# Optimization experiments

Measured on AMD Instinct MI355X. Metric: run time of the kernel, lower is better.

The kernel has to match this reference:

```python
import jax, jax.numpy as jnp
import numpy as np

V, DW, D, H, F, N = 50272, 512, 1024, 16, 4096, 4   # vocab, word_embed_proj_dim, hidden, heads, ffn, layers
B, L = 4, 1024
T = B * L
MAX_POS = 2048


def layernorm(x, w, b, eps=1e-5):
    m = jnp.mean(x, axis=-1, keepdims=True)
    v = jnp.mean((x - m) ** 2, axis=-1, keepdims=True)
    return (x - m) * jax.lax.rsqrt(v + eps) * w + b


def setup_inputs() -> dict:
    key = jax.random.key(0)
    ks = jax.random.split(key, 16)
    s = 0.02
    inp = {
        "input_ids": jax.random.randint(ks[0], (T,), 0, V),
        "positions": jnp.tile(jnp.arange(L), B),          # per-sequence positions 0..L-1
        "offsets": (jnp.arange(B) + 1) * L,               # cumulative sequence ends
        "cache_indices": jnp.arange(T),
        "k_cache": jnp.zeros((N, T, D), jnp.float32),
        "v_cache": jnp.zeros((N, T, D), jnp.float32),
        "embed_w": jax.random.normal(ks[1], (V, DW)) * s,
        "pos_w": jax.random.normal(ks[2], (MAX_POS + 2, D)) * s,
        "proj_in_w": jax.random.normal(ks[3], (D, DW)) * s,
        "proj_out_w": jax.random.normal(ks[4], (DW, D)) * s,
        "ln1_w": jnp.ones((N, D)), "ln1_b": jnp.zeros((N, D)),
        "qw": jax.random.normal(ks[5], (N, D, D)) * s, "qb": jnp.zeros((N, D)),
        "kw": jax.random.normal(ks[6], (N, D, D)) * s, "kb": jnp.zeros((N, D)),
        "vw": jax.random.normal(ks[7], (N, D, D)) * s, "vb": jnp.zeros((N, D)),
        "ow": jax.random.normal(ks[8], (N, D, D)) * s, "ob": jnp.zeros((N, D)),
        "fc1w": jax.random.normal(ks[9], (N, F, D)) * s, "fc1b": jnp.zeros((N, F)),
        "fc2w": jax.random.normal(ks[10], (N, D, F)) * s, "fc2b": jnp.zeros((N, D)),
        "ln2_w": jnp.ones((N, D)), "ln2_b": jnp.zeros((N, D)),
    }
    return inp


def reference(input_ids, positions, offsets, cache_indices, k_cache, v_cache,
              embed_w, pos_w, proj_in_w, proj_out_w,
              ln1_w, ln1_b, qw, qb, kw, kb, vw, vb, ow, ob,
              fc1w, fc1b, fc2w, fc2b, ln2_w, ln2_b):
    # prompt_init=True path: fresh causal varlen attention over packed equal-length sequences.
    hd = D // H
    scale = hd ** -0.5
    emb = embed_w[input_ids] @ proj_in_w.T            # [T, D] (proj_in since DW != D)
    pos = pos_w[positions + 2]                        # learned pos emb with offset 2
    h = (emb + pos).reshape(B, L, D)
    causal = jnp.tril(jnp.ones((L, L), bool))

    def step(h, p):
        l1w, l1b, Wq, bq, Wk, bk, Wv, bv, Wo, bo, W1, b1, W2, b2, l2w, l2b = p
        r = h                                          # post-LN (do_layer_norm_before=False)
        q = (h @ Wq.T + bq).reshape(B, L, H, hd)
        k = (h @ Wk.T + bk).reshape(B, L, H, hd)
        v = (h @ Wv.T + bv).reshape(B, L, H, hd)
        s = jnp.einsum('bqhd,bkhd->bhqk', q * scale, k)
        s = jnp.where(causal, s, -1e9)
        pa = jax.nn.softmax(s, axis=-1)
        o = jnp.einsum('bhqk,bkhd->bqhd', pa, v).reshape(B, L, D)
        h = layernorm(r + (o @ Wo.T + bo), l1w, l1b)
        r = h
        h = jax.nn.relu(h @ W1.T + b1)
        h = h @ W2.T + b2
        h = layernorm(r + h, l2w, l2b)
        return h, None

    h, _ = jax.lax.scan(step, h, (ln1_w, ln1_b, qw, qb, kw, kb, vw, vb, ow, ob,
                                  fc1w, fc1b, fc2w, fc2b, ln2_w, ln2_b))
    # no decoder final_layer_norm when do_layer_norm_before=False
    h = h.reshape(T, D) @ proj_out_w.T                # [T, DW]
    last = h[offsets - 1]                             # last token of each sequence [B, DW]
    return last @ embed_w.T                           # logits [B, V]
```

## Files before the change

### kernel.cpp

```cpp
#include <hip/hip_runtime.h>
#include <stdint.h>

typedef _Float16 f16;
typedef __attribute__((ext_vector_type(8))) _Float16 f16x8;
typedef __attribute__((ext_vector_type(4))) _Float16 f16x4;
typedef __attribute__((ext_vector_type(4))) float f32x4;

constexpr int kT = 4096;
constexpr int kD = 1024;
constexpr int kDW = 512;
constexpr int kF = 4096;
constexpr int kV = 50272;

__device__ __forceinline__ void gload16(const void* g, void* lbase, int lane) {
#if __has_builtin(__builtin_amdgcn_global_load_lds)
  __builtin_amdgcn_global_load_lds((const __attribute__((address_space(1))) void*)g,
                                   (__attribute__((address_space(3))) void*)lbase, 16, 0, 0);
#else
  *(f16x8*)((char*)lbase + lane * 16) = *(const f16x8*)g;
#endif
}

__global__ __launch_bounds__(512, 4) void gemm_p8(
    const f16* __restrict__ A, const f16* __restrict__ W,
    const float* __restrict__ bias, void* __restrict__ Cv,
    int M, int N, int K, int ldc, int flags, int S)
{
  __shared__ f16 LA[2][128 * 64];
  __shared__ f16 LB[2][128 * 64];
  const int tid = threadIdx.x, lane = tid & 63, wv = tid >> 6;
  const int nby = M >> 7;
  const int nb = nby * (N >> 7);
  int id = blockIdx.x;
  id = (id & 7) * ((int)gridDim.x >> 3) + (id >> 3);
  const int s = id / nb;
  const int r = id - s * nb;
  const int bx = r / nby, by = r - bx * nby;
  const int row0 = by * 128, col0 = bx * 128;
  const int klen = K / S, koff = s * klen;
  const int wm = (wv >> 1) * 32, wn = (wv & 1) * 64;
  const int l15 = lane & 15, l4 = lane >> 4;

  f32x4 acc[2][4] = {};

  const int srow = wv * 16 + (lane >> 3);
  const int schunk = ((lane & 7) ^ (lane >> 3)) * 8;
  const f16* Ag = A + (size_t)(row0 + srow) * K + koff + schunk;
  const f16* Wg = W + (size_t)(col0 + srow) * K + koff + schunk;
  const int lrow = wv * 16;

  const int nt = klen >> 6;
#pragma unroll
  for (int j = 0; j < 2; ++j) {
    gload16(Ag + (size_t)j * 8 * K, &LA[0][(lrow + j * 8) * 64], lane);
    gload16(Wg + (size_t)j * 8 * K, &LB[0][(lrow + j * 8) * 64], lane);
  }

  for (int t = 0; t < nt; ++t) {
    const int cur = t & 1;
    if (t + 1 < nt) {
      const size_t ko = (size_t)(t + 1) * 64;
#pragma unroll
      for (int j = 0; j < 2; ++j) {
        gload16(Ag + (size_t)j * 8 * K + ko, &LA[cur ^ 1][(lrow + j * 8) * 64], lane);
        gload16(Wg + (size_t)j * 8 * K + ko, &LB[cur ^ 1][(lrow + j * 8) * 64], lane);
      }
      asm volatile("s_waitcnt vmcnt(4)" ::: "memory");
    } else {
      asm volatile("s_waitcnt vmcnt(0)" ::: "memory");
    }
    __builtin_amdgcn_s_barrier();

    f16x8 af[2][2], bf[2][4];
#pragma unroll
    for (int ks = 0; ks < 2; ++ks) {
#pragma unroll
      for (int mr = 0; mr < 2; ++mr) {
        const int rowa = wm + mr * 16 + l15;
        const int csw = (((ks * 4 + l4) ^ (rowa & 7)) * 8);
        af[ks][mr] = *(const f16x8*)&LA[cur][rowa * 64 + csw];
      }
#pragma unroll
      for (int nr = 0; nr < 4; ++nr) {
        const int rowb = wn + nr * 16 + l15;
        const int csw = (((ks * 4 + l4) ^ (rowb & 7)) * 8);
        bf[ks][nr] = *(const f16x8*)&LB[cur][rowb * 64 + csw];
      }
    }
#pragma unroll
    for (int mr = 0; mr < 2; ++mr)
#pragma unroll
      for (int nr = 0; nr < 4; ++nr) {
        acc[mr][nr] = __builtin_amdgcn_mfma_f32_16x16x32_f16(af[0][mr], bf[0][nr], acc[mr][nr], 0, 0, 0);
        acc[mr][nr] = __builtin_amdgcn_mfma_f32_16x16x32_f16(af[1][mr], bf[1][nr], acc[mr][nr], 0, 0, 0);
      }
    __builtin_amdgcn_sched_barrier(0);
    __builtin_amdgcn_s_barrier();
  }

  const bool relu = (flags & 1) != 0;
  const bool outf = (flags & 2) != 0;
  float* Cf = (float*)Cv + (size_t)s * M * ldc;
  f16* Ch = (f16*)Cv;
  const float* bs = (s == 0) ? bias : nullptr;
#pragma unroll
  for (int nr = 0; nr < 4; ++nr) {
    const int col = col0 + wn + nr * 16 + l15;
    const float bv = bs ? bs[col] : 0.f;
#pragma unroll
    for (int mr = 0; mr < 2; ++mr) {
#pragma unroll
      for (int rr = 0; rr < 4; ++rr) {
        const int row = row0 + wm + mr * 16 + l4 * 4 + rr;
        float v = acc[mr][nr][rr] + bv;
        if (relu) v = fmaxf(v, 0.f);
        if (outf) Cf[(size_t)row * ldc + col] = v;
        else      Ch[(size_t)row * ldc + col] = (f16)v;
      }
    }
  }
}

__global__ __launch_bounds__(256) void gemm_f16(
    const f16* __restrict__ A, const float* __restrict__ W,
    const float* __restrict__ bias, void* __restrict__ Cv,
    int M, int N, int K, int ldc, int flags)
{
  __shared__ f16 As[128][40];
  __shared__ f16 Ws[128][40];
  const int tid = threadIdx.x;
  const int lane = tid & 63;
  const int wid = tid >> 6;
  const int row0 = blockIdx.y * 128, col0 = blockIdx.x * 128;
  const int wm = (wid >> 1) * 64, wn = (wid & 1) * 64;
  const int l15 = lane & 15, k8 = (lane >> 4) * 8;
  const int lr = tid >> 2, lc8 = (tid & 3) * 8;

  f32x4 acc[4][4] = {};

  const f16* Ap = A + (size_t)(row0 + lr) * K + lc8;
  const float* Wp = W + (size_t)(col0 + lr) * K + lc8;

  for (int k0 = 0; k0 < K; k0 += 32) {
    f16x8 a0 = *(const f16x8*)(Ap + k0);
    f16x8 a1 = *(const f16x8*)(Ap + (size_t)64 * K + k0);
    f32x4 w00 = *(const f32x4*)(Wp + k0);
    f32x4 w01 = *(const f32x4*)(Wp + k0 + 4);
    f32x4 w10 = *(const f32x4*)(Wp + (size_t)64 * K + k0);
    f32x4 w11 = *(const f32x4*)(Wp + (size_t)64 * K + k0 + 4);
    f16x8 wv0, wv1;
#pragma unroll
    for (int j = 0; j < 4; ++j) {
      wv0[j] = (f16)w00[j]; wv0[4 + j] = (f16)w01[j];
      wv1[j] = (f16)w10[j]; wv1[4 + j] = (f16)w11[j];
    }
    __syncthreads();
    *(f16x8*)&As[lr][lc8] = a0;
    *(f16x8*)&As[lr + 64][lc8] = a1;
    *(f16x8*)&Ws[lr][lc8] = wv0;
    *(f16x8*)&Ws[lr + 64][lc8] = wv1;
    __syncthreads();
    f16x8 af[4], bfr[4];
#pragma unroll
    for (int r = 0; r < 4; ++r) af[r] = *(const f16x8*)&As[wm + r * 16 + l15][k8];
#pragma unroll
    for (int r = 0; r < 4; ++r) bfr[r] = *(const f16x8*)&Ws[wn + r * 16 + l15][k8];
#pragma unroll
    for (int mr = 0; mr < 4; ++mr)
#pragma unroll
      for (int nr = 0; nr < 4; ++nr)
        acc[mr][nr] = __builtin_amdgcn_mfma_f32_16x16x32_f16(af[mr], bfr[nr], acc[mr][nr], 0, 0, 0);
  }

  const bool relu = (flags & 1) != 0;
  const bool outf = (flags & 2) != 0;
  float* Cf = (float*)Cv;
  f16* Ch = (f16*)Cv;
#pragma unroll
  for (int nr = 0; nr < 4; ++nr) {
    const int col = col0 + wn + nr * 16 + l15;
    const float bv = bias ? bias[col] : 0.f;
#pragma unroll
    for (int mr = 0; mr < 4; ++mr) {
#pragma unroll
      for (int r = 0; r < 4; ++r) {
        const int row = row0 + wm + mr * 16 + (lane >> 4) * 4 + r;
        float v = acc[mr][nr][r] + bv;
        if (relu) v = fmaxf(v, 0.f);
        if (outf) Cf[(size_t)row * ldc + col] = v;
        else      Ch[(size_t)row * ldc + col] = (f16)v;
      }
    }
  }
}

__global__ __launch_bounds__(256) void attn_mfma(const f16* __restrict__ qkv,
                                                 f16* __restrict__ out)
{
  __shared__ f16 Ks[64][72];
  __shared__ f16 Vt[64][72];
  __shared__ f16 Ps[4][16][72];
  const int qt = blockIdx.x, h = blockIdx.y, b = blockIdx.z;
  const int tid = threadIdx.x, lane = tid & 63, wv = tid >> 6;
  const int l15 = lane & 15, l4 = lane >> 4;

  const size_t qrow = (size_t)(b * 1024 + qt * 64 + wv * 16 + l15);
  const f16* qp = qkv + qrow * 3072 + h * 64 + l4 * 8;
  const f16x8 qa0 = *(const f16x8*)qp;
  const f16x8 qa1 = *(const f16x8*)(qp + 32);

  float m[4] = {-1e30f, -1e30f, -1e30f, -1e30f};
  float l[4] = {0.f, 0.f, 0.f, 0.f};
  f32x4 o[4] = {};

  const int skey = tid >> 2;
  const int spart = (tid & 3) * 16;

  for (int kt = 0; kt <= qt; ++kt) {
    __syncthreads();
    {
      const f16* kvb = qkv + (size_t)(b * 1024 + kt * 64 + skey) * 3072 + h * 64;
      f16x8 kk0 = *(const f16x8*)(kvb + 1024 + spart);
      f16x8 kk1 = *(const f16x8*)(kvb + 1024 + spart + 8);
      f16x8 vv0 = *(const f16x8*)(kvb + 2048 + spart);
      f16x8 vv1 = *(const f16x8*)(kvb + 2048 + spart + 8);
      *(f16x8*)&Ks[skey][spart] = kk0;
      *(f16x8*)&Ks[skey][spart + 8] = kk1;
#pragma unroll
      for (int j = 0; j < 8; ++j) {
        Vt[spart + j][skey] = vv0[j];
        Vt[spart + 8 + j][skey] = vv1[j];
      }
    }
    __syncthreads();

    f32x4 s[4] = {};
#pragma unroll
    for (int f = 0; f < 4; ++f) {
      f16x8 kb0 = *(const f16x8*)&Ks[f * 16 + l15][l4 * 8];
      f16x8 kb1 = *(const f16x8*)&Ks[f * 16 + l15][32 + l4 * 8];
      s[f] = __builtin_amdgcn_mfma_f32_16x16x32_f16(qa0, kb0, s[f], 0, 0, 0);
      s[f] = __builtin_amdgcn_mfma_f32_16x16x32_f16(qa1, kb1, s[f], 0, 0, 0);
    }
    float sc[4][4];
    if (kt == qt) {
#pragma unroll
      for (int f = 0; f < 4; ++f)
#pragma unroll
        for (int r = 0; r < 4; ++r) {
          const int qg = wv * 16 + l4 * 4 + r;
          const int kg = f * 16 + l15;
          sc[f][r] = (kg <= qg) ? s[f][r] * 0.125f : -1e9f;
        }
    } else {
#pragma unroll
      for (int f = 0; f < 4; ++f)
#pragma unroll
        for (int r = 0; r < 4; ++r) sc[f][r] = s[f][r] * 0.125f;
    }
    float corr[4];
#pragma unroll
    for (int r = 0; r < 4; ++r) {
      float tm = fmaxf(fmaxf(sc[0][r], sc[1][r]), fmaxf(sc[2][r], sc[3][r]));
      tm = fmaxf(tm, __shfl_xor(tm, 1));
      tm = fmaxf(tm, __shfl_xor(tm, 2));
      tm = fmaxf(tm, __shfl_xor(tm, 4));
      tm = fmaxf(tm, __shfl_xor(tm, 8));
      const float mn = fmaxf(m[r], tm);
      corr[r] = __expf(m[r] - mn);
      float ps = 0.f;
#pragma unroll
      for (int f = 0; f < 4; ++f) { sc[f][r] = __expf(sc[f][r] - mn); ps += sc[f][r]; }
      ps += __shfl_xor(ps, 1);
      ps += __shfl_xor(ps, 2);
      ps += __shfl_xor(ps, 4);
      ps += __shfl_xor(ps, 8);
      l[r] = l[r] * corr[r] + ps;
      m[r] = mn;
    }
#pragma unroll
    for (int f = 0; f < 4; ++f)
#pragma unroll
      for (int r = 0; r < 4; ++r)
        Ps[wv][l4 * 4 + r][f * 16 + l15] = (f16)sc[f][r];
#pragma unroll
    for (int hf = 0; hf < 4; ++hf)
#pragma unroll
      for (int r = 0; r < 4; ++r) o[hf][r] *= corr[r];
    f16x8 pa0 = *(const f16x8*)&Ps[wv][l15][l4 * 8];
    f16x8 pa1 = *(const f16x8*)&Ps[wv][l15][32 + l4 * 8];
#pragma unroll
    for (int hf = 0; hf < 4; ++hf) {
      f16x8 vb0 = *(const f16x8*)&Vt[hf * 16 + l15][l4 * 8];
      f16x8 vb1 = *(const f16x8*)&Vt[hf * 16 + l15][32 + l4 * 8];
      o[hf] = __builtin_amdgcn_mfma_f32_16x16x32_f16(pa0, vb0, o[hf], 0, 0, 0);
      o[hf] = __builtin_amdgcn_mfma_f32_16x16x32_f16(pa1, vb1, o[hf], 0, 0, 0);
    }
  }

  float inv[4];
#pragma unroll
  for (int r = 0; r < 4; ++r) inv[r] = 1.f / l[r];
  f16* dst = out + (size_t)(b * 1024 + qt * 64 + wv * 16 + l4 * 4) * 1024 + h * 64 + l15;
#pragma unroll
  for (int hf = 0; hf < 4; ++hf)
#pragma unroll
    for (int r = 0; r < 4; ++r)
      dst[(size_t)r * 1024 + hf * 16] = (f16)(o[hf][r] * inv[r]);
}

__global__ __launch_bounds__(256) void add_ln3(
    const float* __restrict__ R, const float* __restrict__ X1,
    const float* __restrict__ X2,
    const float* __restrict__ w, const float* __restrict__ bvec,
    float* __restrict__ O32, f16* __restrict__ Oh)
{
  const int row = blockIdx.x, tid = threadIdx.x;
  const size_t base = (size_t)row * 1024 + tid * 4;
  f32x4 v = *(const f32x4*)&R[base];
  v += *(const f32x4*)&X1[base];
  v += *(const f32x4*)&X2[base];
  float sm = v[0] + v[1] + v[2] + v[3];
  float sq = v[0] * v[0] + v[1] * v[1] + v[2] * v[2] + v[3] * v[3];
#pragma unroll
  for (int msk = 32; msk; msk >>= 1) { sm += __shfl_xor(sm, msk); sq += __shfl_xor(sq, msk); }
  __shared__ float sb[4], qb_[4];
  const int wid = tid >> 6, lane = tid & 63;
  if (lane == 0) { sb[wid] = sm; qb_[wid] = sq; }
  __syncthreads();
  sm = sb[0] + sb[1] + sb[2] + sb[3];
  sq = qb_[0] + qb_[1] + qb_[2] + qb_[3];
  const float mean = sm * (1.f / 1024.f);
  const float var = sq * (1.f / 1024.f) - mean * mean;
  const float rstd = rsqrtf(var + 1e-5f);
  const f32x4 w4 = *(const f32x4*)&w[tid * 4];
  const f32x4 b4 = *(const f32x4*)&bvec[tid * 4];
  f32x4 y;
  f16x4 yh;
#pragma unroll
  for (int j = 0; j < 4; ++j) {
    y[j] = (v[j] - mean) * rstd * w4[j] + b4[j];
    yh[j] = (f16)y[j];
  }
  *(f32x4*)&O32[base] = y;
  *(f16x4*)&Oh[base] = yh;
}

__global__ __launch_bounds__(256) void add_ln(
    const float* __restrict__ R, const float* __restrict__ X,
    const float* __restrict__ w, const float* __restrict__ bvec,
    float* __restrict__ O32, f16* __restrict__ Oh)
{
  const int row = blockIdx.x, tid = threadIdx.x;
  const size_t base = (size_t)row * 1024 + tid * 4;
  f32x4 v = *(const f32x4*)&R[base];
  v += *(const f32x4*)&X[base];
  float sm = v[0] + v[1] + v[2] + v[3];
  float sq = v[0] * v[0] + v[1] * v[1] + v[2] * v[2] + v[3] * v[3];
#pragma unroll
  for (int msk = 32; msk; msk >>= 1) { sm += __shfl_xor(sm, msk); sq += __shfl_xor(sq, msk); }
  __shared__ float sb[4], qb_[4];
  const int wid = tid >> 6, lane = tid & 63;
  if (lane == 0) { sb[wid] = sm; qb_[wid] = sq; }
  __syncthreads();
  sm = sb[0] + sb[1] + sb[2] + sb[3];
  sq = qb_[0] + qb_[1] + qb_[2] + qb_[3];
  const float mean = sm * (1.f / 1024.f);
  const float var = sq * (1.f / 1024.f) - mean * mean;
  const float rstd = rsqrtf(var + 1e-5f);
  const f32x4 w4 = *(const f32x4*)&w[tid * 4];
  const f32x4 b4 = *(const f32x4*)&bvec[tid * 4];
  f32x4 y;
  f16x4 yh;
#pragma unroll
  for (int j = 0; j < 4; ++j) {
    y[j] = (v[j] - mean) * rstd * w4[j] + b4[j];
    yh[j] = (f16)y[j];
  }
  *(f32x4*)&O32[base] = y;
  *(f16x4*)&Oh[base] = yh;
}

__global__ __launch_bounds__(256) void gather_embed(
    const int* __restrict__ ids, const float* __restrict__ ew, f16* __restrict__ E)
{
  const int idx = blockIdx.x * 256 + threadIdx.x;
  const int t = idx >> 6, c = (idx & 63) * 8;
  const float* src = ew + (size_t)ids[t] * 512 + c;
  f32x4 f0 = *(const f32x4*)src, f1 = *(const f32x4*)(src + 4);
  f16x8 o_;
#pragma unroll
  for (int j = 0; j < 4; ++j) { o_[j] = (f16)f0[j]; o_[4 + j] = (f16)f1[j]; }
  *(f16x8*)(E + (size_t)t * 512 + c) = o_;
}

__global__ __launch_bounds__(256) void pos_add2(
    const float* __restrict__ X1, const float* __restrict__ X2,
    const float* __restrict__ posw,
    const int* __restrict__ positions, float* __restrict__ H32, f16* __restrict__ Hh)
{
  const int idx = blockIdx.x * 256 + threadIdx.x;
  const int t = idx >> 7, c = (idx & 127) * 8;
  const size_t base = (size_t)t * 1024 + c;
  const float* pp = posw + (size_t)(positions[t] + 2) * 1024 + c;
  f32x4 a0 = *(const f32x4*)&X1[base];
  f32x4 a1 = *(const f32x4*)&X1[base + 4];
  a0 += *(const f32x4*)&X2[base];
  a1 += *(const f32x4*)&X2[base + 4];
  a0 += *(const f32x4*)pp;
  a1 += *(const f32x4*)(pp + 4);
  f16x8 hh;
#pragma unroll
  for (int j = 0; j < 4; ++j) { hh[j] = (f16)a0[j]; hh[4 + j] = (f16)a1[j]; }
  *(f32x4*)&H32[base] = a0;
  *(f32x4*)&H32[base + 4] = a1;
  *(f16x8*)&Hh[base] = hh;
}

__global__ __launch_bounds__(256) void pos_add(
    const float* __restrict__ X, const float* __restrict__ posw,
    const int* __restrict__ positions, float* __restrict__ H32, f16* __restrict__ Hh)
{
  const int idx = blockIdx.x * 256 + threadIdx.x;
  const int t = idx >> 7, c = (idx & 127) * 8;
  const float* xp = X + (size_t)t * 1024 + c;
  const float* pp = posw + (size_t)(positions[t] + 2) * 1024 + c;
  f32x4 a0 = *(const f32x4*)xp, a1 = *(const f32x4*)(xp + 4);
  a0 += *(const f32x4*)pp;
  a1 += *(const f32x4*)(pp + 4);
  f16x8 hh;
#pragma unroll
  for (int j = 0; j < 4; ++j) { hh[j] = (f16)a0[j]; hh[4 + j] = (f16)a1[j]; }
  *(f32x4*)&H32[(size_t)t * 1024 + c] = a0;
  *(f32x4*)&H32[(size_t)t * 1024 + c + 4] = a1;
  *(f16x8*)&Hh[(size_t)t * 1024 + c] = hh;
}

__global__ __launch_bounds__(256) void last_proj(
    const float* __restrict__ H32, const float* __restrict__ pw,
    const int* __restrict__ offs, float* __restrict__ y)
{
  const int o = blockIdx.x * 4 + (threadIdx.x >> 6), lane = threadIdx.x & 63;
  const int b = o >> 9, w = o & 511;
  const int row = offs[b] - 1;
  const float* hp = H32 + (size_t)row * 1024;
  const float* wp = pw + (size_t)w * 1024;
  float s = 0.f;
#pragma unroll
  for (int j = 0; j < 4; ++j) {
    f32x4 hv = *(const f32x4*)&hp[(lane + 64 * j) * 4];
    f32x4 wv = *(const f32x4*)&wp[(lane + 64 * j) * 4];
    s += hv[0] * wv[0] + hv[1] * wv[1] + hv[2] * wv[2] + hv[3] * wv[3];
  }
#pragma unroll
  for (int msk = 32; msk; msk >>= 1) s += __shfl_xor(s, msk);
  if (lane == 0) y[o] = s;
}

__global__ __launch_bounds__(256) void logits4(const float* __restrict__ y,
                                               const float* __restrict__ ew,
                                               float* __restrict__ out)
{
  __shared__ float ys[2048];
  const int tid = threadIdx.x;
  ((f32x4*)ys)[tid] = ((const f32x4*)y)[tid];
  ((f32x4*)ys)[tid + 256] = ((const f32x4*)y)[tid + 256];
  __syncthreads();
  const int v = blockIdx.x * 4 + (tid >> 6);
  const int lane = tid & 63;
  const float* wp = ew + (size_t)v * 512 + lane * 8;
  const f32x4 e0 = *(const f32x4*)wp;
  const f32x4 e1 = *(const f32x4*)(wp + 4);
  float s0 = 0.f, s1 = 0.f, s2 = 0.f, s3 = 0.f;
#pragma unroll
  for (int j = 0; j < 4; ++j) {
    const int c0 = lane * 8 + j, c1 = lane * 8 + 4 + j;
    s0 += e0[j] * ys[c0] + e1[j] * ys[c1];
    s1 += e0[j] * ys[512 + c0] + e1[j] * ys[512 + c1];
    s2 += e0[j] * ys[1024 + c0] + e1[j] * ys[1024 + c1];
    s3 += e0[j] * ys[1536 + c0] + e1[j] * ys[1536 + c1];
  }
#pragma unroll
  for (int msk = 32; msk; msk >>= 1) {
    s0 += __shfl_xor(s0, msk); s1 += __shfl_xor(s1, msk);
    s2 += __shfl_xor(s2, msk); s3 += __shfl_xor(s3, msk);
  }
  if (lane == 0) {
    out[v] = s0;
    out[50272 + v] = s1;
    out[2 * 50272 + v] = s2;
    out[3 * 50272 + v] = s3;
  }
}

__global__ __launch_bounds__(256) void conv_f16(const float* __restrict__ s,
                                                f16* __restrict__ d, int n8)
{
  const int i = blockIdx.x * 256 + threadIdx.x;
  if (i >= n8) return;
  const f32x4 a = *(const f32x4*)(s + (size_t)i * 8);
  const f32x4 b = *(const f32x4*)(s + (size_t)i * 8 + 4);
  f16x8 o_;
#pragma unroll
  for (int j = 0; j < 4; ++j) { o_[j] = (f16)a[j]; o_[4 + j] = (f16)b[j]; }
  *(f16x8*)(d + (size_t)i * 8) = o_;
}

__global__ __launch_bounds__(256) void qkvw_pack(const float* __restrict__ qw,
                                                 const float* __restrict__ kw,
                                                 const float* __restrict__ vw,
                                                 f16* __restrict__ dst)
{
  const size_t i = (size_t)(blockIdx.x * 256 + threadIdx.x) * 8;
  const size_t li = i / 3145728;
  const size_t r = i - li * 3145728;
  const int mt = (int)(r >> 20);
  const size_t c = r & 1048575;
  const float* s = (mt == 0 ? qw : (mt == 1 ? kw : vw)) + li * 1048576 + c;
  const f32x4 a = *(const f32x4*)s;
  const f32x4 b = *(const f32x4*)(s + 4);
  f16x8 o_;
#pragma unroll
  for (int j = 0; j < 4; ++j) { o_[j] = (f16)a[j]; o_[4 + j] = (f16)b[j]; }
  *(f16x8*)(dst + i) = o_;
}

__global__ __launch_bounds__(256) void qkvb_pack(const float* __restrict__ qb,
                                                 const float* __restrict__ kb,
                                                 const float* __restrict__ vb,
                                                 float* __restrict__ dst)
{
  const int i = blockIdx.x * 256 + threadIdx.x;
  const int li = i / 3072;
  const int r = i - li * 3072;
  const int mt = r >> 10;
  const int c = r & 1023;
  const float* s = (mt == 0 ? qb : (mt == 1 ? kb : vb));
  dst[i] = s[li * 1024 + c];
}

extern "C" void kernel_launch(void* const* d_in, const int* in_sizes, int n_in,
                              void* d_out, int out_size, void* d_ws, size_t ws_size,
                              hipStream_t stream)
{
  const int* ids        = (const int*)d_in[0];
  const int* positions  = (const int*)d_in[1];
  const int* offs       = (const int*)d_in[2];
  const float* embed_w    = (const float*)d_in[6];
  const float* pos_w      = (const float*)d_in[7];
  const float* proj_in_w  = (const float*)d_in[8];
  const float* proj_out_w = (const float*)d_in[9];
  const float* ln1w = (const float*)d_in[10];
  const float* ln1b = (const float*)d_in[11];
  const float* qw   = (const float*)d_in[12];
  const float* qb   = (const float*)d_in[13];
  const float* kw   = (const float*)d_in[14];
  const float* kb   = (const float*)d_in[15];
  const float* vw   = (const float*)d_in[16];
  const float* vb   = (const float*)d_in[17];
  const float* ow   = (const float*)d_in[18];
  const float* ob   = (const float*)d_in[19];
  const float* fc1w = (const float*)d_in[20];
  const float* fc1b = (const float*)d_in[21];
  const float* fc2w = (const float*)d_in[22];
  const float* fc2b = (const float*)d_in[23];
  const float* ln2w = (const float*)d_in[24];
  const float* ln2b = (const float*)d_in[25];

  char* ws = (char*)d_ws;
  size_t off = 0;
  auto take = [&](size_t bytes) -> char* {
    char* p = ws + off;
    off += (bytes + 255) & ~(size_t)255;
    return p;
  };
  f16*   E   = (f16*)  take((size_t)kT * kDW * 2);
  float* h32 = (float*)take((size_t)kT * kD * 4);
  f16*   hbf = (f16*)  take((size_t)kT * kD * 2);
  f16*   qkv = (f16*)  take((size_t)kT * 3072 * 2);
  f16*   att = (f16*)  take((size_t)kT * kD * 2);
  f16*   t1  = (f16*)  take((size_t)kT * kF * 2);
  float* t2  = (float*)take((size_t)kT * kD * 4 * 2);
  float* yb  = (float*)take((size_t)4 * kDW * 4);
  f16*   pw_in = (f16*)take((size_t)kD * kDW * 2);
  f16*   qkvw  = (f16*)take((size_t)4 * 3072 * kD * 2);
  f16*   oww   = (f16*)take((size_t)4 * kD * kD * 2);
  f16*   f1w   = (f16*)take((size_t)4 * kF * kD * 2);
  f16*   f2w   = (f16*)take((size_t)4 * kD * kF * 2);
  float* qkvb  = (float*)take((size_t)4 * 3072 * 4);
  const bool wok = (off <= ws_size);
  float* t2b = t2 + (size_t)kT * kD;
  (void)in_sizes; (void)n_in; (void)out_size;

  const dim3 blk(256);
  const dim3 blk8(512);
  const dim3 gD(kD / 128, kT / 128);
  const dim3 gF(kF / 128, kT / 128);
  const dim3 gAtt(16, 16, 4);
  const int nbD   = (kD / 128) * (kT / 128);
  const int nbQKV = (3072 / 128) * (kT / 128);
  const int nbF   = (kF / 128) * (kT / 128);

  if (wok) {
    conv_f16<<<256, blk, 0, stream>>>(proj_in_w, pw_in, 65536);
    qkvw_pack<<<6144, blk, 0, stream>>>(qw, kw, vw, qkvw);
    conv_f16<<<2048, blk, 0, stream>>>(ow, oww, 524288);
    conv_f16<<<8192, blk, 0, stream>>>(fc1w, f1w, 2097152);
    conv_f16<<<8192, blk, 0, stream>>>(fc2w, f2w, 2097152);
    qkvb_pack<<<48, blk, 0, stream>>>(qb, kb, vb, qkvb);
  }

  gather_embed<<<1024, blk, 0, stream>>>(ids, embed_w, E);
  if (wok) {
    gemm_p8<<<nbD * 2, blk8, 0, stream>>>(E, pw_in, nullptr, t2, kT, kD, kDW, kD, 2, 2);
    pos_add2<<<2048, blk, 0, stream>>>(t2, t2b, pos_w, positions, h32, hbf);
  } else {
    gemm_f16<<<gD, blk, 0, stream>>>(E, proj_in_w, nullptr, t2, kT, kD, kDW, kD, 2);
    pos_add<<<2048, blk, 0, stream>>>(t2, pos_w, positions, h32, hbf);
  }

  for (int n = 0; n < 4; ++n) {
    const size_t wo = (size_t)n * kD * kD;
    if (wok) {
      gemm_p8<<<nbQKV, blk8, 0, stream>>>(hbf, qkvw + (size_t)n * 3145728, qkvb + n * 3072,
                                          qkv, kT, 3072, kD, 3072, 0, 1);
      attn_mfma<<<gAtt, blk, 0, stream>>>(qkv, att);
      gemm_p8<<<nbD * 2, blk8, 0, stream>>>(att, oww + wo, ob + n * kD, t2, kT, kD, kD, kD, 2, 2);
      add_ln3<<<kT, blk, 0, stream>>>(h32, t2, t2b, ln1w + n * kD, ln1b + n * kD, h32, hbf);
      gemm_p8<<<nbF, blk8, 0, stream>>>(hbf, f1w + (size_t)n * kF * kD, fc1b + n * kF, t1, kT, kF, kD, kF, 1, 1);
      gemm_p8<<<nbD * 2, blk8, 0, stream>>>(t1, f2w + (size_t)n * kD * kF, fc2b + n * kD, t2, kT, kD, kF, kD, 2, 2);
      add_ln3<<<kT, blk, 0, stream>>>(h32, t2, t2b, ln2w + n * kD, ln2b + n * kD, h32, hbf);
    } else {
      gemm_f16<<<gD, blk, 0, stream>>>(hbf, qw + wo, qb + n * kD, qkv + 0,    kT, kD, kD, 3072, 0);
      gemm_f16<<<gD, blk, 0, stream>>>(hbf, kw + wo, kb + n * kD, qkv + 1024, kT, kD, kD, 3072, 0);
      gemm_f16<<<gD, blk, 0, stream>>>(hbf, vw + wo, vb + n * kD, qkv + 2048, kT, kD, kD, 3072, 0);
      attn_mfma<<<gAtt, blk, 0, stream>>>(qkv, att);
      gemm_f16<<<gD, blk, 0, stream>>>(att, ow + wo, ob + n * kD, t2, kT, kD, kD, kD, 2);
      add_ln<<<kT, blk, 0, stream>>>(h32, t2, ln1w + n * kD, ln1b + n * kD, h32, hbf);
      gemm_f16<<<gF, blk, 0, stream>>>(hbf, fc1w + (size_t)n * kF * kD, fc1b + n * kF, t1, kT, kF, kD, kF, 1);
      gemm_f16<<<gD, blk, 0, stream>>>(t1, fc2w + (size_t)n * kD * kF, fc2b + n * kD, t2, kT, kD, kF, kD, 2);
      add_ln<<<kT, blk, 0, stream>>>(h32, t2, ln2w + n * kD, ln2b + n * kD, h32, hbf);
    }
  }

  last_proj<<<512, blk, 0, stream>>>(h32, proj_out_w, offs, yb);
  logits4<<<12568, blk, 0, stream>>>(yb, embed_w, (float*)d_out);
}
```

Before: 1.202 ms.

## Enlarge attention query tile to 128 rows and swizzle transposed V in LDS

The attention kernel now handles 128 query rows per block, with each wave owning 32 rows as two MFMA row groups. Each K/V tile loaded into shared memory is reused by twice as many queries, which halves K/V global traffic and launches half as many blocks. The transposed V tile gets an XOR swizzle on its column index to reduce LDS bank conflicts. In exchange, causal work is less balanced across waves because some waves skip tiles while others compute, and register pressure rises.

```diff
diff --git a/kernel.cpp b/kernel.cpp
--- a/kernel.cpp
+++ b/kernel.cpp
@@ -194,29 +194,40 @@
   }
 }
 
-__global__ __launch_bounds__(256) void attn_mfma(const f16* __restrict__ qkv,
-                                                 f16* __restrict__ out)
+__global__ __launch_bounds__(256) void attn_mfma2(const f16* __restrict__ qkv,
+                                                  f16* __restrict__ out)
 {
   __shared__ f16 Ks[64][72];
   __shared__ f16 Vt[64][72];
-  __shared__ f16 Ps[4][16][72];
+  __shared__ f16 Ps[4][32][72];
   const int qt = blockIdx.x, h = blockIdx.y, b = blockIdx.z;
   const int tid = threadIdx.x, lane = tid & 63, wv = tid >> 6;
   const int l15 = lane & 15, l4 = lane >> 4;
 
-  const size_t qrow = (size_t)(b * 1024 + qt * 64 + wv * 16 + l15);
-  const f16* qp = qkv + qrow * 3072 + h * 64 + l4 * 8;
-  const f16x8 qa0 = *(const f16x8*)qp;
-  const f16x8 qa1 = *(const f16x8*)(qp + 32);
-
-  float m[4] = {-1e30f, -1e30f, -1e30f, -1e30f};
-  float l[4] = {0.f, 0.f, 0.f, 0.f};
-  f32x4 o[4] = {};
+  f16x8 qa[2][2];
+#pragma unroll
+  for (int mr = 0; mr < 2; ++mr) {
+    const size_t qrow = (size_t)(b * 1024 + qt * 128 + wv * 32 + mr * 16 + l15);
+#pragma unroll
+    for (int ks = 0; ks < 2; ++ks)
+      qa[mr][ks] = *(const f16x8*)(qkv + qrow * 3072 + h * 64 + ks * 32 + l4 * 8);
+  }
+
+  float m[2][4], l[2][4];
+#pragma unroll
+  for (int mr = 0; mr < 2; ++mr)
+#pragma unroll
+    for (int r = 0; r < 4; ++r) { m[mr][r] = -1e30f; l[mr][r] = 0.f; }
+  f32x4 o[2][4] = {};
 
   const int skey = tid >> 2;
   const int spart = (tid & 3) * 16;
-
-  for (int kt = 0; kt <= qt; ++kt) {
+  const int vxor = (skey >> 3) ^ (tid & 3);
+  const int vcol = vxor * 8 + (skey & 7);
+  const int qmin = qt * 128 + wv * 32;
+  const int ntiles = 2 * qt + 2;
+
+  for (int kt = 0; kt < ntiles; ++kt) {
     __syncthreads();
     {
       const f16* kvb = qkv + (size_t)(b * 1024 + kt * 64 + skey) * 3072 + h * 64;
@@ -228,85 +239,104 @@
       *(f16x8*)&Ks[skey][spart + 8] = kk1;
 #pragma unroll
       for (int j = 0; j < 8; ++j) {
-        Vt[spart + j][skey] = vv0[j];
-        Vt[spart + 8 + j][skey] = vv1[j];
+        Vt[spart + j][vcol] = vv0[j];
+        Vt[spart + 8 + j][vcol] = vv1[j];
       }
     }
     __syncthreads();
 
-    f32x4 s[4] = {};
-#pragma unroll
-    for (int f = 0; f < 4; ++f) {
-      f16x8 kb0 = *(const f16x8*)&Ks[f * 16 + l15][l4 * 8];
-      f16x8 kb1 = *(const f16x8*)&Ks[f * 16 + l15][32 + l4 * 8];
-      s[f] = __builtin_amdgcn_mfma_f32_16x16x32_f16(qa0, kb0, s[f], 0, 0, 0);
-      s[f] = __builtin_amdgcn_mfma_f32_16x16x32_f16(qa1, kb1, s[f], 0, 0, 0);
-    }
-    float sc[4][4];
-    if (kt == qt) {
-#pragma unroll
-      for (int f = 0; f < 4; ++f)
+    if (kt * 64 <= qmin + 31) {
+      f32x4 s[2][4] = {};
+#pragma unroll
+      for (int f = 0; f < 4; ++f) {
+        f16x8 kb0 = *(const f16x8*)&Ks[f * 16 + l15][l4 * 8];
+        f16x8 kb1 = *(const f16x8*)&Ks[f * 16 + l15][32 + l4 * 8];
+#pragma unroll
+        for (int mr = 0; mr < 2; ++mr) {
+          s[mr][f] = __builtin_amdgcn_mfma_f32_16x16x32_f16(qa[mr][0], kb0, s[mr][f], 0, 0, 0);
+          s[mr][f] = __builtin_amdgcn_mfma_f32_16x16x32_f16(qa[mr][1], kb1, s[mr][f], 0, 0, 0);
+        }
+      }
+#pragma unroll
+      for (int mr = 0; mr < 2; ++mr) {
+        float sc[4][4];
+        const bool needmask = (kt * 64 + 63) > (qmin + mr * 16);
+        if (needmask) {
+#pragma unroll
+          for (int f = 0; f < 4; ++f)
+#pragma unroll
+            for (int r = 0; r < 4; ++r) {
+              const int qg = qmin + mr * 16 + l4 * 4 + r;
+              const int kg = kt * 64 + f * 16 + l15;
+              sc[f][r] = (kg <= qg) ? s[mr][f][r] * 0.125f : -1e9f;
+            }
+        } else {
+#pragma unroll
+          for (int f = 0; f < 4; ++f)
+#pragma unroll
+            for (int r = 0; r < 4; ++r) sc[f][r] = s[mr][f][r] * 0.125f;
+        }
+        float corr[4];
 #pragma unroll
         for (int r = 0; r < 4; ++r) {
-          const int qg = wv * 16 + l4 * 4 + r;
-          const int kg = f * 16 + l15;
-          sc[f][r] = (kg <= qg) ? s[f][r] * 0.125f : -1e9f;
+          float tm = fmaxf(fmaxf(sc[0][r], sc[1][r]), fmaxf(sc[2][r], sc[3][r]));
+          tm = fmaxf(tm, __shfl_xor(tm, 1));
+          tm = fmaxf(tm, __shfl_xor(tm, 2));
+          tm = fmaxf(tm, __shfl_xor(tm, 4));
+          tm = fmaxf(tm, __shfl_xor(tm, 8));
+          const float mn = fmaxf(m[mr][r], tm);
+          corr[r] = __expf(m[mr][r] - mn);
+          float ps = 0.f;
+#pragma unroll
+          for (int f = 0; f < 4; ++f) { sc[f][r] = __expf(sc[f][r] - mn); ps += sc[f][r]; }
+          ps += __shfl_xor(ps, 1);
+          ps += __shfl_xor(ps, 2);
+          ps += __shfl_xor(ps, 4);
+          ps += __shfl_xor(ps, 8);
+          l[mr][r] = l[mr][r] * corr[r] + ps;
+          m[mr][r] = mn;
         }
-    } else {
-#pragma unroll
-      for (int f = 0; f < 4; ++f)
-#pragma unroll
-        for (int r = 0; r < 4; ++r) sc[f][r] = s[f][r] * 0.125f;
-    }
-    float corr[4];
-#pragma unroll
-    for (int r = 0; r < 4; ++r) {
-      float tm = fmaxf(fmaxf(sc[0][r], sc[1][r]), fmaxf(sc[2][r], sc[3][r]));
-      tm = fmaxf(tm, __shfl_xor(tm, 1));
-      tm = fmaxf(tm, __shfl_xor(tm, 2));
-      tm = fmaxf(tm, __shfl_xor(tm, 4));
-      tm = fmaxf(tm, __shfl_xor(tm, 8));
-      const float mn = fmaxf(m[r], tm);
-      corr[r] = __expf(m[r] - mn);
-      float ps = 0.f;
-#pragma unroll
-      for (int f = 0; f < 4; ++f) { sc[f][r] = __expf(sc[f][r] - mn); ps += sc[f][r]; }
-      ps += __shfl_xor(ps, 1);
-      ps += __shfl_xor(ps, 2);
-      ps += __shfl_xor(ps, 4);
-      ps += __shfl_xor(ps, 8);
-      l[r] = l[r] * corr[r] + ps;
-      m[r] = mn;
-    }
-#pragma unroll
-    for (int f = 0; f < 4; ++f)
+#pragma unroll
+        for (int f = 0; f < 4; ++f)
+#pragma unroll
+          for (int r = 0; r < 4; ++r)
+            Ps[wv][mr * 16 + l4 * 4 + r][f * 16 + l15] = (f16)sc[f][r];
+#pragma unroll
+        for (int hf = 0; hf < 4; ++hf)
+#pragma unroll
+          for (int r = 0; r < 4; ++r) o[mr][hf][r] *= corr[r];
+      }
+      f16x8 pa[2][2];
+#pragma unroll
+      for (int mr = 0; mr < 2; ++mr)
+#pragma unroll
+        for (int ks = 0; ks < 2; ++ks)
+          pa[mr][ks] = *(const f16x8*)&Ps[wv][mr * 16 + l15][ks * 32 + l4 * 8];
+#pragma unroll
+      for (int hf = 0; hf < 4; ++hf) {
+        f16x8 vb0 = *(const f16x8*)&Vt[hf * 16 + l15][((l4) ^ hf) * 8];
+        f16x8 vb1 = *(const f16x8*)&Vt[hf * 16 + l15][((4 + l4) ^ hf) * 8];
+#pragma unroll
+        for (int mr = 0; mr < 2; ++mr) {
+          o[mr][hf] = __builtin_amdgcn_mfma_f32_16x16x32_f16(pa[mr][0], vb0, o[mr][hf], 0, 0, 0);
+          o[mr][hf] = __builtin_amdgcn_mfma_f32_16x16x32_f16(pa[mr][1], vb1, o[mr][hf], 0, 0, 0);
+        }
+      }
+    }
+  }
+
+#pragma unroll
+  for (int mr = 0; mr < 2; ++mr) {
+    float inv[4];
+#pragma unroll
+    for (int r = 0; r < 4; ++r) inv[r] = 1.f / l[mr][r];
+    f16* dst = out + (size_t)(b * 1024 + qt * 128 + wv * 32 + mr * 16 + l4 * 4) * 1024 + h * 64 + l15;
+#pragma unroll
+    for (int hf = 0; hf < 4; ++hf)
 #pragma unroll
       for (int r = 0; r < 4; ++r)
-        Ps[wv][l4 * 4 + r][f * 16 + l15] = (f16)sc[f][r];
-#pragma unroll
-    for (int hf = 0; hf < 4; ++hf)
-#pragma unroll
-      for (int r = 0; r < 4; ++r) o[hf][r] *= corr[r];
-    f16x8 pa0 = *(const f16x8*)&Ps[wv][l15][l4 * 8];
-    f16x8 pa1 = *(const f16x8*)&Ps[wv][l15][32 + l4 * 8];
-#pragma unroll
-    for (int hf = 0; hf < 4; ++hf) {
-      f16x8 vb0 = *(const f16x8*)&Vt[hf * 16 + l15][l4 * 8];
-      f16x8 vb1 = *(const f16x8*)&Vt[hf * 16 + l15][32 + l4 * 8];
-      o[hf] = __builtin_amdgcn_mfma_f32_16x16x32_f16(pa0, vb0, o[hf], 0, 0, 0);
-      o[hf] = __builtin_amdgcn_mfma_f32_16x16x32_f16(pa1, vb1, o[hf], 0, 0, 0);
-    }
-  }
-
-  float inv[4];
-#pragma unroll
-  for (int r = 0; r < 4; ++r) inv[r] = 1.f / l[r];
-  f16* dst = out + (size_t)(b * 1024 + qt * 64 + wv * 16 + l4 * 4) * 1024 + h * 64 + l15;
-#pragma unroll
-  for (int hf = 0; hf < 4; ++hf)
-#pragma unroll
-    for (int r = 0; r < 4; ++r)
-      dst[(size_t)r * 1024 + hf * 16] = (f16)(o[hf][r] * inv[r]);
+        dst[(size_t)r * 1024 + hf * 16] = (f16)(o[mr][hf][r] * inv[r]);
+  }
 }
 
 __global__ __launch_bounds__(256) void add_ln3(
@@ -597,6 +627,7 @@
   const dim3 gD(kD / 128, kT / 128);
   const dim3 gF(kF / 128, kT / 128);
   const dim3 gAtt(16, 16, 4);
+  const dim3 gAtt2(8, 16, 4);
   const int nbD   = (kD / 128) * (kT / 128);
   const int nbQKV = (3072 / 128) * (kT / 128);
   const int nbF   = (kF / 128) * (kT / 128);
@@ -624,7 +655,7 @@
     if (wok) {
       gemm_p8<<<nbQKV, blk8, 0, stream>>>(hbf, qkvw + (size_t)n * 3145728, qkvb + n * 3072,
                                           qkv, kT, 3072, kD, 3072, 0, 1);
-      attn_mfma<<<gAtt, blk, 0, stream>>>(qkv, att);
+      attn_mfma2<<<gAtt2, blk, 0, stream>>>(qkv, att);
       gemm_p8<<<nbD * 2, blk8, 0, stream>>>(att, oww + wo, ob + n * kD, t2, kT, kD, kD, kD, 2, 2);
       add_ln3<<<kT, blk, 0, stream>>>(h32, t2, t2b, ln1w + n * kD, ln1b + n * kD, h32, hbf);
       gemm_p8<<<nbF, blk8, 0, stream>>>(hbf, f1w + (size_t)n * kF * kD, fc1b + n * kF, t1, kT, kF, kD, kF, 1, 1);
@@ -634,7 +665,7 @@
       gemm_f16<<<gD, blk, 0, stream>>>(hbf, qw + wo, qb + n * kD, qkv + 0,    kT, kD, kD, 3072, 0);
       gemm_f16<<<gD, blk, 0, stream>>>(hbf, kw + wo, kb + n * kD, qkv + 1024, kT, kD, kD, 3072, 0);
       gemm_f16<<<gD, blk, 0, stream>>>(hbf, vw + wo, vb + n * kD, qkv + 2048, kT, kD, kD, 3072, 0);
-      attn_mfma<<<gAtt, blk, 0, stream>>>(qkv, att);
+      attn_mfma2<<<gAtt2, blk, 0, stream>>>(qkv, att);
       gemm_f16<<<gD, blk, 0, stream>>>(att, ow + wo, ob + n * kD, t2, kT, kD, kD, kD, 2);
       add_ln<<<kT, blk, 0, stream>>>(h32, t2, ln1w + n * kD, ln1b + n * kD, h32, hbf);
       gemm_f16<<<gF, blk, 0, stream>>>(hbf, fc1w + (size_t)n * kF * kD, fc1b + n * kF, t1, kT, kF, kD, kF, 1);
```

Measured after the change: 1.174 ms. 2.3% less time.
